# Optimization experiments

Hardware: AMD Instinct MI355X
Metric: run time of the kernel (lower is better)

The kernel has to match this reference:

```python
import jax, jax.numpy as jnp
import numpy as np

BITS = 4
GROUP = 128
M, K, N = 16, 4096, 11008


def setup_inputs() -> dict:
    key = jax.random.key(0)
    k1, k2, k3 = jax.random.split(key, 3)
    A = jax.random.normal(k1, (M, K), dtype=jnp.float16)
    # packed 4-bit weights: 2 nibbles per byte, stored as int32 holding 0..255
    qweight = jax.random.randint(k2, (N, K * BITS // 8), 0, 256, dtype=jnp.int32)
    # small positive-ish scales like real GPTQ checkpoints
    scales = (jax.random.normal(k3, (N, K // GROUP)) * 0.01 + 0.02).astype(jnp.float16)
    zeros = jnp.zeros((N, K // GROUP), dtype=jnp.float16)
    bias = jnp.zeros((N,), dtype=jnp.float16)
    return {"A": A, "qweight": qweight, "scales": scales, "zeros": zeros, "bias": bias}


def _dequant(qweight, scales, zeros):
    # qweight: (N, K//2) packed; element idx -> byte idx//2, low nibble if idx even
    low = qweight & 0xF
    high = (qweight >> 4) & 0xF
    w_int = jnp.stack([low, high], axis=-1).reshape(qweight.shape[0], -1)  # (N, K)
    # per-group dequant with 'original' zeros: W = (q - z) * s
    s = jnp.repeat(scales, GROUP, axis=1)  # (N, K)
    z = jnp.repeat(zeros, GROUP, axis=1)   # (N, K)
    return (w_int.astype(jnp.float16) - z) * s


def reference(A, qweight, scales, zeros, bias):
    W = _dequant(qweight, scales, zeros)           # (N, K) fp16
    return jnp.matmul(A, W.T) + bias               # (M, N) fp16
```

## Files before the change

kernel.cpp:

```cpp
#include <hip/hip_runtime.h>

#define KK 4096
#define NN 11008
#define GRP 128
#define KW (KK / 2)
#define NGRP (KK / GRP)
#define KSPLIT 4

using short8  = __attribute__((ext_vector_type(8))) short;
using float4v = __attribute__((ext_vector_type(4))) float;

static __device__ __forceinline__ unsigned int pack_bf16(float lo, float hi) {
    unsigned int ul = __builtin_bit_cast(unsigned int, lo);
    unsigned int uh = __builtin_bit_cast(unsigned int, hi);
    ul = (ul + 0x7FFFu + ((ul >> 16) & 1u)) >> 16;
    uh = (uh + 0x7FFFu + ((uh >> 16) & 1u)) & 0xFFFF0000u;
    return ul | uh;
}

__global__ __launch_bounds__(256) void qgemm_kernel(
    const float* __restrict__ A,
    const int*   __restrict__ qweight,
    const float* __restrict__ scales,
    const float* __restrict__ zeros,
    const float* __restrict__ bias,
    float*       __restrict__ out)
{
    const int n0   = blockIdx.x * 16;
    const int wid  = threadIdx.x >> 6;
    const int lane = threadIdx.x & 63;
    const int nl   = lane & 15;
    const int quad = lane >> 4;
    const int n    = n0 + nl;

    const int kbase = wid * (KK / KSPLIT);

    float4v acc = {0.f, 0.f, 0.f, 0.f};

    const int*   qrow  = qweight + (size_t)n * KW;
    const float* Arowf = A + (size_t)nl * KK;

    for (int g = 0; g < (KK / KSPLIT) / GRP; ++g) {
        const int grp = (kbase >> 7) + g;
        const float s_f = scales[n * NGRP + grp];
        const float z_f = zeros[n * NGRP + grp];
        const float c_f = -(128.0f + z_f) * s_f;

        #pragma unroll
        for (int t = 0; t < 4; ++t) {
            const int k0 = kbase + g * GRP + t * 32 + quad * 8;

            float4v a0 = *(const float4v*)(Arowf + k0);
            float4v a1 = *(const float4v*)(Arowf + k0 + 4);
            union { short8 s8; unsigned int u[4]; } af;
            af.u[0] = pack_bf16(a0[0], a0[1]);
            af.u[1] = pack_bf16(a0[2], a0[3]);
            af.u[2] = pack_bf16(a1[0], a1[1]);
            af.u[3] = pack_bf16(a1[2], a1[3]);

            int4 w4 = *(const int4*)(qrow + (k0 >> 1));
            const unsigned int ws[4] = {(unsigned int)w4.x, (unsigned int)w4.y,
                                        (unsigned int)w4.z, (unsigned int)w4.w};
            union { short8 s8; unsigned int u[4]; } b;
            #pragma unroll
            for (int i = 0; i < 4; ++i) {
                unsigned int u = (ws[i] & 0xFu) | ((ws[i] << 12) & 0x000F0000u)
                               | 0x43004300u;
                float flo = __builtin_bit_cast(float, u << 16);
                float fhi = __builtin_bit_cast(float, u & 0xFFFF0000u);
                float dlo = __builtin_fmaf(flo, s_f, c_f);
                float dhi = __builtin_fmaf(fhi, s_f, c_f);
                b.u[i] = pack_bf16(dlo, dhi);
            }
            acc = __builtin_amdgcn_mfma_f32_16x16x32_bf16(af.s8, b.s8, acc, 0, 0, 0);
        }
    }

    __shared__ float red[KSPLIT][16][16];
    #pragma unroll
    for (int r = 0; r < 4; ++r)
        red[wid][quad * 4 + r][nl] = acc[r];
    __syncthreads();

    const int t  = threadIdx.x;
    const int m  = t >> 4;
    const int nn = t & 15;
    float sum = red[0][m][nn] + red[1][m][nn] + red[2][m][nn] + red[3][m][nn];
    sum += bias[n0 + nn];
    out[(size_t)m * NN + n0 + nn] = sum;
}

extern "C" void kernel_launch(void* const* d_in, const int* in_sizes, int n_in,
                              void* d_out, int out_size, void* d_ws, size_t ws_size,
                              hipStream_t stream) {
    const float* A       = (const float*)d_in[0];
    const int*   qweight = (const int*)d_in[1];
    const float* scales  = (const float*)d_in[2];
    const float* zeros   = (const float*)d_in[3];
    const float* bias    = (const float*)d_in[4];
    float*       out     = (float*)d_out;

    qgemm_kernel<<<dim3(NN / 16), dim3(256), 0, stream>>>(
        A, qweight, scales, zeros, bias, out);
}
```

Baseline: 162.2 us.

## Double K-split waves per block and batch loads ahead of dequant

Raises the per-block K split from 4 to 8 waves (512 threads), so each wave covers 512 K elements and more waves are in flight per CU to hide memory latency. Inside each group, all four A and weight loads are issued before any conversion or MFMA, which raises memory-level parallelism per wave. The final reduction now sums 8 partials and only half the threads write output. The cost is more register pressure from the batched loads, a larger shared reduction buffer, and fewer iterations per wave to amortize setup.

Measured after the change: 155.5 us. -4.1%, faster.

```diff
diff --git a/kernel.cpp b/kernel.cpp
--- a/kernel.cpp
+++ b/kernel.cpp
@@ -5,7 +5,7 @@
 #define GRP 128
 #define KW (KK / 2)
 #define NGRP (KK / GRP)
-#define KSPLIT 4
+#define KSPLIT 8
 
 using short8  = __attribute__((ext_vector_type(8))) short;
 using float4v = __attribute__((ext_vector_type(4))) float;
@@ -18,7 +18,7 @@
     return ul | uh;
 }
 
-__global__ __launch_bounds__(256) void qgemm_kernel(
+__global__ __launch_bounds__(512) void qgemm_kernel(
     const float* __restrict__ A,
     const int*   __restrict__ qweight,
     const float* __restrict__ scales,
@@ -40,27 +40,33 @@
     const int*   qrow  = qweight + (size_t)n * KW;
     const float* Arowf = A + (size_t)nl * KK;
 
+    #pragma unroll
     for (int g = 0; g < (KK / KSPLIT) / GRP; ++g) {
         const int grp = (kbase >> 7) + g;
         const float s_f = scales[n * NGRP + grp];
         const float z_f = zeros[n * NGRP + grp];
         const float c_f = -(128.0f + z_f) * s_f;
 
+        float4v a0[4], a1[4];
+        int4    w4[4];
         #pragma unroll
         for (int t = 0; t < 4; ++t) {
             const int k0 = kbase + g * GRP + t * 32 + quad * 8;
+            a0[t] = *(const float4v*)(Arowf + k0);
+            a1[t] = *(const float4v*)(Arowf + k0 + 4);
+            w4[t] = *(const int4*)(qrow + (k0 >> 1));
+        }
 
-            float4v a0 = *(const float4v*)(Arowf + k0);
-            float4v a1 = *(const float4v*)(Arowf + k0 + 4);
+        #pragma unroll
+        for (int t = 0; t < 4; ++t) {
             union { short8 s8; unsigned int u[4]; } af;
-            af.u[0] = pack_bf16(a0[0], a0[1]);
-            af.u[1] = pack_bf16(a0[2], a0[3]);
-            af.u[2] = pack_bf16(a1[0], a1[1]);
-            af.u[3] = pack_bf16(a1[2], a1[3]);
+            af.u[0] = pack_bf16(a0[t][0], a0[t][1]);
+            af.u[1] = pack_bf16(a0[t][2], a0[t][3]);
+            af.u[2] = pack_bf16(a1[t][0], a1[t][1]);
+            af.u[3] = pack_bf16(a1[t][2], a1[t][3]);
 
-            int4 w4 = *(const int4*)(qrow + (k0 >> 1));
-            const unsigned int ws[4] = {(unsigned int)w4.x, (unsigned int)w4.y,
-                                        (unsigned int)w4.z, (unsigned int)w4.w};
+            const unsigned int ws[4] = {(unsigned int)w4[t].x, (unsigned int)w4[t].y,
+                                        (unsigned int)w4[t].z, (unsigned int)w4[t].w};
             union { short8 s8; unsigned int u[4]; } b;
             #pragma unroll
             for (int i = 0; i < 4; ++i) {
@@ -82,12 +88,16 @@
         red[wid][quad * 4 + r][nl] = acc[r];
     __syncthreads();
 
-    const int t  = threadIdx.x;
-    const int m  = t >> 4;
-    const int nn = t & 15;
-    float sum = red[0][m][nn] + red[1][m][nn] + red[2][m][nn] + red[3][m][nn];
-    sum += bias[n0 + nn];
-    out[(size_t)m * NN + n0 + nn] = sum;
+    const int t = threadIdx.x;
+    if (t < 256) {
+        const int m  = t >> 4;
+        const int nn = t & 15;
+        float sum = 0.f;
+        #pragma unroll
+        for (int w = 0; w < KSPLIT; ++w) sum += red[w][m][nn];
+        sum += bias[n0 + nn];
+        out[(size_t)m * NN + n0 + nn] = sum;
+    }
 }
 
 extern "C" void kernel_launch(void* const* d_in, const int* in_sizes, int n_in,
@@ -100,6 +110,6 @@
     const float* bias    = (const float*)d_in[4];
     float*       out     = (float*)d_out;
 
-    qgemm_kernel<<<dim3(NN / 16), dim3(256), 0, stream>>>(
+    qgemm_kernel<<<dim3(NN / 16), dim3(512), 0, stream>>>(
         A, qweight, scales, zeros, bias, out);
 }
```
